# Optimization experiments

Measured on AMD Instinct MI355X. Metric: run time of the kernel, lower is better.

Reference implementation:

```python
import jax, jax.numpy as jnp
import numpy as np

D_MODEL = 1024
MAX_SEQ_LEN = 8192
B, S = 16, 8192
D_HALF = D_MODEL // 2
LN_EPS = 1e-5


def _spine(max_len=MAX_SEQ_LEN):
    s = [0, 2, 4]
    while s[-1] < max_len:
        nv = 2 * s[-1] + 2 * s[-2] + 2 * s[-3]
        if nv < max_len:
            s.append(nv)
        else:
            break
    return jnp.asarray(s, dtype=jnp.int32)


def _sinusoidal_pe(max_len=MAX_SEQ_LEN, dm=D_HALF):
    pe = np.zeros((max_len, dm), dtype=np.float32)
    pos = np.arange(max_len, dtype=np.float32)[:, None]
    div = np.exp(np.arange(0, dm, 2, dtype=np.float32) * -(np.log(10000.0) / dm))
    pe[:, 0::2] = np.sin(pos * div)
    pe[:, 1::2] = np.cos(pos * div)
    return jnp.asarray(pe)


def setup_inputs() -> dict:
    key = jax.random.key(0)
    k1, k2, k3 = jax.random.split(key, 3)
    positions = jax.random.randint(k1, (B, S), 0, MAX_SEQ_LEN).astype(jnp.int32)
    pe = _sinusoidal_pe()  # [max_seq_len, d_model//2] buffer
    W1 = jax.random.normal(k2, (D_HALF, 3), dtype=jnp.float32) * 0.3  # Linear(3, d_half) weight
    b1 = jax.random.normal(k3, (D_HALF,), dtype=jnp.float32) * 0.1
    ln_gamma = jnp.ones((D_HALF,), dtype=jnp.float32)
    ln_beta = jnp.zeros((D_HALF,), dtype=jnp.float32)
    return {"positions": positions, "pe": pe, "W1": W1, "b1": b1,
            "ln_gamma": ln_gamma, "ln_beta": ln_beta}


def _lattice_features(positions, spine):
    # level = number of spine entries <= pos (searchsorted right); spine[0]==0 so level >= 1
    level = jnp.searchsorted(spine, positions.astype(jnp.int32), side='right')  # [B,S]
    n = spine.shape[0]
    left_dist = positions.astype(jnp.int32) - spine[level - 1]
    right_idx = jnp.minimum(level, n - 1)
    right_dist = jnp.where(level < n, spine[right_idx] - positions.astype(jnp.int32), 0)
    return jnp.stack([left_dist, right_dist, level], axis=-1).astype(jnp.float32)  # [B,S,3]


def reference(positions, pe, W1, b1, ln_gamma, ln_beta):
    spine = _spine()
    abs_enc = pe[positions]                      # [B,S,d_half] gather
    feats = _lattice_features(positions, spine)  # [B,S,3]
    h = jnp.einsum('bsk,dk->bsd', feats, W1) + b1  # Linear(3, d_half)
    mu = jnp.mean(h, axis=-1, keepdims=True)
    var = jnp.mean(jnp.square(h - mu), axis=-1, keepdims=True)
    h = (h - mu) * jax.lax.rsqrt(var + LN_EPS) * ln_gamma + ln_beta
    lat_enc = jax.nn.gelu(h, approximate=False)  # torch GELU default = exact erf
    return jnp.concatenate([abs_enc, lat_enc], axis=-1)  # [B,S,d_model]
```

## Files before the change

kernel.cpp:

```cpp
#include <hip/hip_runtime.h>
#include <math.h>

#define D_HALF 512
#define D_MODEL 1024
#define MAX_SEQ 8192

__device__ __forceinline__ void pos_feats(int pos, float& f0, float& f1, float& f2) {
  constexpr int spine[10] = {0, 2, 4, 12, 36, 104, 304, 888, 2592, 7568};
  int lev = 1;
  int left_base = 0;
#pragma unroll
  for (int i = 1; i < 10; ++i) {
    if (pos >= spine[i]) { lev++; left_base = spine[i]; }
  }
  int right = 0;
#pragma unroll
  for (int i = 9; i >= 1; --i) {
    if (pos < spine[i]) right = spine[i] - pos;
  }
  f0 = (float)(pos - left_base);
  f1 = (float)right;
  f2 = (float)lev;
}

__device__ __forceinline__ float4 lat_quad(int pos, int t,
    const float* __restrict__ W1, const float* __restrict__ b1,
    const float* __restrict__ gamma, const float* __restrict__ beta,
    const float* __restrict__ stats)
{
  float f0, f1, f2;
  pos_feats(pos, f0, f1, f2);
  const float m0 = stats[0], m1 = stats[1], m2 = stats[2], m3 = stats[3];
  const float C00 = stats[4],  C01 = stats[5],  C02 = stats[6],  C03 = stats[7];
  const float C11 = stats[8],  C12 = stats[9],  C13 = stats[10];
  const float C22 = stats[11], C23 = stats[12], C33 = stats[13];

  const float mu  = fmaf(m0, f0, fmaf(m1, f1, fmaf(m2, f2, m3)));
  const float var = C33
                  + f0 * (C00 * f0 + 2.0f * (C01 * f1 + C02 * f2 + C03))
                  + f1 * (C11 * f1 + 2.0f * (C12 * f2 + C13))
                  + f2 * (C22 * f2 + 2.0f * C23);
  const float rstd = rsqrtf(var + 1e-5f);

  const int d = 4 * t;
  const float4* wv = (const float4*)(W1 + 3 * d);
  const float4 wa = wv[0], wb = wv[1], wc = wv[2];
  const float4 bb = ((const float4*)b1)[t];
  const float4 gg = ((const float4*)gamma)[t];
  const float4 be = ((const float4*)beta)[t];

  const float h0 = fmaf(wa.x, f0, fmaf(wa.y, f1, fmaf(wa.z, f2, bb.x)));
  const float h1 = fmaf(wa.w, f0, fmaf(wb.x, f1, fmaf(wb.y, f2, bb.y)));
  const float h2 = fmaf(wb.z, f0, fmaf(wb.w, f1, fmaf(wc.x, f2, bb.z)));
  const float h3 = fmaf(wc.y, f0, fmaf(wc.z, f1, fmaf(wc.w, f2, bb.w)));

  const float x0 = fmaf((h0 - mu) * rstd, gg.x, be.x);
  const float x1 = fmaf((h1 - mu) * rstd, gg.y, be.y);
  const float x2 = fmaf((h2 - mu) * rstd, gg.z, be.z);
  const float x3 = fmaf((h3 - mu) * rstd, gg.w, be.w);

  const float is2 = 0.70710678118654752440f;
  float4 r;
  r.x = 0.5f * x0 * (1.0f + erff(x0 * is2));
  r.y = 0.5f * x1 * (1.0f + erff(x1 * is2));
  r.z = 0.5f * x2 * (1.0f + erff(x2 * is2));
  r.w = 0.5f * x3 * (1.0f + erff(x3 * is2));
  return r;
}

__global__ __launch_bounds__(256) void lattice_stats(
    const float* __restrict__ W1, const float* __restrict__ b1,
    float* __restrict__ stats)
{
  const int t = threadIdx.x;
  float s[4] = {0.f, 0.f, 0.f, 0.f};
  float p[10] = {0.f, 0.f, 0.f, 0.f, 0.f, 0.f, 0.f, 0.f, 0.f, 0.f};
  for (int d = t; d < D_HALF; d += 256) {
    const float w0 = W1[3 * d], w1 = W1[3 * d + 1], w2 = W1[3 * d + 2], bb = b1[d];
    s[0] += w0; s[1] += w1; s[2] += w2; s[3] += bb;
    p[0] += w0 * w0; p[1] += w0 * w1; p[2] += w0 * w2; p[3] += w0 * bb;
    p[4] += w1 * w1; p[5] += w1 * w2; p[6] += w1 * bb;
    p[7] += w2 * w2; p[8] += w2 * bb; p[9] += bb * bb;
  }
  float vals[14] = {s[0], s[1], s[2], s[3], p[0], p[1], p[2], p[3], p[4],
                    p[5], p[6], p[7], p[8], p[9]};
#pragma unroll
  for (int i = 0; i < 14; ++i) {
    float v = vals[i];
#pragma unroll
    for (int off = 32; off > 0; off >>= 1) v += __shfl_down(v, off, 64);
    vals[i] = v;
  }
  __shared__ float sm[4][14];
  const int wave = t >> 6, lane = t & 63;
  if (lane == 0) {
#pragma unroll
    for (int i = 0; i < 14; ++i) sm[wave][i] = vals[i];
  }
  __syncthreads();
  if (t == 0) {
    float tot[14];
#pragma unroll
    for (int i = 0; i < 14; ++i) tot[i] = sm[0][i] + sm[1][i] + sm[2][i] + sm[3][i];
    const float inv = 1.0f / (float)D_HALF;
    const float m0 = tot[0] * inv, m1 = tot[1] * inv, m2 = tot[2] * inv, m3 = tot[3] * inv;
    stats[0] = m0; stats[1] = m1; stats[2] = m2; stats[3] = m3;
    stats[4]  = tot[4]  * inv - m0 * m0;
    stats[5]  = tot[5]  * inv - m0 * m1;
    stats[6]  = tot[6]  * inv - m0 * m2;
    stats[7]  = tot[7]  * inv - m0 * m3;
    stats[8]  = tot[8]  * inv - m1 * m1;
    stats[9]  = tot[9]  * inv - m1 * m2;
    stats[10] = tot[10] * inv - m1 * m3;
    stats[11] = tot[11] * inv - m2 * m2;
    stats[12] = tot[12] * inv - m2 * m3;
    stats[13] = tot[13] * inv - m3 * m3;
  }
}

__global__ __launch_bounds__(256) void lattice_build_table(
    const float* __restrict__ W1, const float* __restrict__ b1,
    const float* __restrict__ gamma, const float* __restrict__ beta,
    const float* __restrict__ stats, float* __restrict__ table)
{
  const int p = blockIdx.x * 2 + threadIdx.y;
  const int t = threadIdx.x;
  float4 r = lat_quad(p, t, W1, b1, gamma, beta, stats);
  ((float4*)(table + (size_t)p * D_HALF))[t] = r;
}

__global__ __launch_bounds__(256) void lattice_gather(
    const int* __restrict__ positions, const float* __restrict__ pe,
    const float* __restrict__ table, float* __restrict__ out)
{
  const int row = blockIdx.x * 2 + threadIdx.y;
  const int t = threadIdx.x;
  const int pos = positions[row];
  const float4 pv = ((const float4*)(pe + (size_t)pos * D_HALF))[t];
  const float4 lv = ((const float4*)(table + (size_t)pos * D_HALF))[t];
  float* outRow = out + (size_t)row * D_MODEL;
  ((float4*)outRow)[t] = pv;
  ((float4*)(outRow + D_HALF))[t] = lv;
}

__global__ __launch_bounds__(256) void lattice_direct(
    const int* __restrict__ positions, const float* __restrict__ pe,
    const float* __restrict__ W1, const float* __restrict__ b1,
    const float* __restrict__ gamma, const float* __restrict__ beta,
    const float* __restrict__ stats, float* __restrict__ out)
{
  const int row = blockIdx.x * 2 + threadIdx.y;
  const int t = threadIdx.x;
  const int pos = positions[row];
  const float4 pv = ((const float4*)(pe + (size_t)pos * D_HALF))[t];
  float4 r = lat_quad(pos, t, W1, b1, gamma, beta, stats);
  float* outRow = out + (size_t)row * D_MODEL;
  ((float4*)outRow)[t] = pv;
  ((float4*)(outRow + D_HALF))[t] = r;
}

extern "C" void kernel_launch(void* const* d_in, const int* in_sizes, int n_in,
                              void* d_out, int out_size, void* d_ws, size_t ws_size,
                              hipStream_t stream) {
  const int*   positions = (const int*)d_in[0];
  const float* pe        = (const float*)d_in[1];
  const float* W1        = (const float*)d_in[2];
  const float* b1        = (const float*)d_in[3];
  const float* ln_gamma  = (const float*)d_in[4];
  const float* ln_beta   = (const float*)d_in[5];
  float* out = (float*)d_out;

  const int rows = in_sizes[0];
  float* stats = (float*)d_ws;
  float* table = (float*)((char*)d_ws + 256);
  const size_t need = 256 + (size_t)MAX_SEQ * D_HALF * sizeof(float);

  hipLaunchKernelGGL(lattice_stats, dim3(1), dim3(256), 0, stream, W1, b1, stats);

  dim3 block(128, 2);
  if (ws_size >= need) {
    hipLaunchKernelGGL(lattice_build_table, dim3(MAX_SEQ / 2), block, 0, stream,
                       W1, b1, ln_gamma, ln_beta, stats, table);
    hipLaunchKernelGGL(lattice_gather, dim3(rows / 2), block, 0, stream,
                       positions, pe, table, out);
  } else {
    hipLaunchKernelGGL(lattice_direct, dim3(rows / 2), block, 0, stream,
                       positions, pe, W1, b1, ln_gamma, ln_beta, stats, out);
  }
}
```

Before: 593.1 us.

## Build combined pe+lattice table and gather full rows with nontemporal stores

The build kernel now writes a combined 8192x1024 table holding the pe row next to the computed lattice encoding. The gather kernel then copies one contiguous 4KB row per output row, 16 rows per block with four loads in flight, and writes with nontemporal stores. This replaces two separate scattered 2KB reads per row and reduces cache pollution from the 512MB output stream. In exchange the workspace must be twice as large (32MB table), and the table build copies pe once more.

```diff
diff --git a/kernel.cpp b/kernel.cpp
--- a/kernel.cpp
+++ b/kernel.cpp
@@ -4,6 +4,8 @@
 #define D_HALF 512
 #define D_MODEL 1024
 #define MAX_SEQ 8192
+
+typedef float vf4 __attribute__((ext_vector_type(4)));
 
 __device__ __forceinline__ void pos_feats(int pos, float& f0, float& f1, float& f2) {
   constexpr int spine[10] = {0, 2, 4, 12, 36, 104, 304, 888, 2592, 7568};
@@ -23,7 +25,7 @@
   f2 = (float)lev;
 }
 
-__device__ __forceinline__ float4 lat_quad(int pos, int t,
+__device__ __forceinline__ vf4 lat_quad(int pos, int t,
     const float* __restrict__ W1, const float* __restrict__ b1,
     const float* __restrict__ gamma, const float* __restrict__ beta,
     const float* __restrict__ stats)
@@ -43,11 +45,11 @@
   const float rstd = rsqrtf(var + 1e-5f);
 
   const int d = 4 * t;
-  const float4* wv = (const float4*)(W1 + 3 * d);
-  const float4 wa = wv[0], wb = wv[1], wc = wv[2];
-  const float4 bb = ((const float4*)b1)[t];
-  const float4 gg = ((const float4*)gamma)[t];
-  const float4 be = ((const float4*)beta)[t];
+  const vf4* wv = (const vf4*)(W1 + 3 * d);
+  const vf4 wa = wv[0], wb = wv[1], wc = wv[2];
+  const vf4 bb = ((const vf4*)b1)[t];
+  const vf4 gg = ((const vf4*)gamma)[t];
+  const vf4 be = ((const vf4*)beta)[t];
 
   const float h0 = fmaf(wa.x, f0, fmaf(wa.y, f1, fmaf(wa.z, f2, bb.x)));
   const float h1 = fmaf(wa.w, f0, fmaf(wb.x, f1, fmaf(wb.y, f2, bb.y)));
@@ -60,7 +62,7 @@
   const float x3 = fmaf((h3 - mu) * rstd, gg.w, be.w);
 
   const float is2 = 0.70710678118654752440f;
-  float4 r;
+  vf4 r;
   r.x = 0.5f * x0 * (1.0f + erff(x0 * is2));
   r.y = 0.5f * x1 * (1.0f + erff(x1 * is2));
   r.z = 0.5f * x2 * (1.0f + erff(x2 * is2));
@@ -118,29 +120,58 @@
   }
 }
 
-__global__ __launch_bounds__(256) void lattice_build_table(
+__global__ __launch_bounds__(256) void lattice_build_combo(
+    const float* __restrict__ pe,
     const float* __restrict__ W1, const float* __restrict__ b1,
     const float* __restrict__ gamma, const float* __restrict__ beta,
-    const float* __restrict__ stats, float* __restrict__ table)
-{
-  const int p = blockIdx.x * 2 + threadIdx.y;
-  const int t = threadIdx.x;
-  float4 r = lat_quad(p, t, W1, b1, gamma, beta, stats);
-  ((float4*)(table + (size_t)p * D_HALF))[t] = r;
-}
-
-__global__ __launch_bounds__(256) void lattice_gather(
-    const int* __restrict__ positions, const float* __restrict__ pe,
-    const float* __restrict__ table, float* __restrict__ out)
-{
-  const int row = blockIdx.x * 2 + threadIdx.y;
-  const int t = threadIdx.x;
-  const int pos = positions[row];
-  const float4 pv = ((const float4*)(pe + (size_t)pos * D_HALF))[t];
-  const float4 lv = ((const float4*)(table + (size_t)pos * D_HALF))[t];
-  float* outRow = out + (size_t)row * D_MODEL;
-  ((float4*)outRow)[t] = pv;
-  ((float4*)(outRow + D_HALF))[t] = lv;
+    const float* __restrict__ stats, float* __restrict__ combo)
+{
+  const int p = blockIdx.x;
+  const int t = threadIdx.x;
+  vf4 v;
+  if (t < 128) {
+    v = ((const vf4*)(pe + (size_t)p * D_HALF))[t];
+  } else {
+    v = lat_quad(p, t - 128, W1, b1, gamma, beta, stats);
+  }
+  ((vf4*)(combo + (size_t)p * D_MODEL))[t] = v;
+}
+
+#define GROWS 16
+__global__ __launch_bounds__(256) void combo_gather(
+    const int* __restrict__ positions, const float* __restrict__ combo,
+    float* __restrict__ out, int rows)
+{
+  const int t = threadIdx.x;
+  const long long row0 = (long long)blockIdx.x * GROWS;
+#pragma unroll
+  for (int r = 0; r < GROWS; r += 4) {
+    const long long rr = row0 + r;
+    if (rr + 3 < rows) {
+      const int p0 = positions[rr + 0];
+      const int p1 = positions[rr + 1];
+      const int p2 = positions[rr + 2];
+      const int p3 = positions[rr + 3];
+      const vf4 a = ((const vf4*)(combo + (size_t)p0 * D_MODEL))[t];
+      const vf4 b = ((const vf4*)(combo + (size_t)p1 * D_MODEL))[t];
+      const vf4 c = ((const vf4*)(combo + (size_t)p2 * D_MODEL))[t];
+      const vf4 d = ((const vf4*)(combo + (size_t)p3 * D_MODEL))[t];
+      __builtin_nontemporal_store(a, ((vf4*)(out + (size_t)(rr + 0) * D_MODEL)) + t);
+      __builtin_nontemporal_store(b, ((vf4*)(out + (size_t)(rr + 1) * D_MODEL)) + t);
+      __builtin_nontemporal_store(c, ((vf4*)(out + (size_t)(rr + 2) * D_MODEL)) + t);
+      __builtin_nontemporal_store(d, ((vf4*)(out + (size_t)(rr + 3) * D_MODEL)) + t);
+    } else {
+#pragma unroll
+      for (int k = 0; k < 4; ++k) {
+        const long long row = rr + k;
+        if (row < rows) {
+          const int p = positions[row];
+          const vf4 v = ((const vf4*)(combo + (size_t)p * D_MODEL))[t];
+          __builtin_nontemporal_store(v, ((vf4*)(out + (size_t)row * D_MODEL)) + t);
+        }
+      }
+    }
+  }
 }
 
 __global__ __launch_bounds__(256) void lattice_direct(
@@ -152,11 +183,11 @@
   const int row = blockIdx.x * 2 + threadIdx.y;
   const int t = threadIdx.x;
   const int pos = positions[row];
-  const float4 pv = ((const float4*)(pe + (size_t)pos * D_HALF))[t];
-  float4 r = lat_quad(pos, t, W1, b1, gamma, beta, stats);
+  const vf4 pv = ((const vf4*)(pe + (size_t)pos * D_HALF))[t];
+  vf4 r = lat_quad(pos, t, W1, b1, gamma, beta, stats);
   float* outRow = out + (size_t)row * D_MODEL;
-  ((float4*)outRow)[t] = pv;
-  ((float4*)(outRow + D_HALF))[t] = r;
+  __builtin_nontemporal_store(pv, ((vf4*)outRow) + t);
+  __builtin_nontemporal_store(r, ((vf4*)(outRow + D_HALF)) + t);
 }
 
 extern "C" void kernel_launch(void* const* d_in, const int* in_sizes, int n_in,
@@ -172,18 +203,19 @@
 
   const int rows = in_sizes[0];
   float* stats = (float*)d_ws;
-  float* table = (float*)((char*)d_ws + 256);
-  const size_t need = 256 + (size_t)MAX_SEQ * D_HALF * sizeof(float);
+  float* combo = (float*)((char*)d_ws + 256);
+  const size_t need = 256 + (size_t)MAX_SEQ * D_MODEL * sizeof(float);
 
   hipLaunchKernelGGL(lattice_stats, dim3(1), dim3(256), 0, stream, W1, b1, stats);
 
-  dim3 block(128, 2);
   if (ws_size >= need) {
-    hipLaunchKernelGGL(lattice_build_table, dim3(MAX_SEQ / 2), block, 0, stream,
-                       W1, b1, ln_gamma, ln_beta, stats, table);
-    hipLaunchKernelGGL(lattice_gather, dim3(rows / 2), block, 0, stream,
-                       positions, pe, table, out);
+    hipLaunchKernelGGL(lattice_build_combo, dim3(MAX_SEQ), dim3(256), 0, stream,
+                       pe, W1, b1, ln_gamma, ln_beta, stats, combo);
+    const int blocks = (rows + GROWS - 1) / GROWS;
+    hipLaunchKernelGGL(combo_gather, dim3(blocks), dim3(256), 0, stream,
+                       positions, combo, out, rows);
   } else {
+    dim3 block(128, 2);
     hipLaunchKernelGGL(lattice_direct, dim3(rows / 2), block, 0, stream,
                        positions, pe, W1, b1, ln_gamma, ln_beta, stats, out);
   }
```

Result: no change. 599.5 us (+1.1%).
